# Kernel tuning notes

Hardware: AMD Instinct MI355X
Metric: run time of the kernel (lower is better)

The kernel has to match this reference:

```python
import jax, jax.numpy as jnp
import numpy as np

HEADS = 8


def setup_inputs() -> dict:
    key = jax.random.key(0)
    ks = jax.random.split(key, 7)
    b, t, e, h = 4, 2048, 128, HEADS
    x = jax.random.normal(ks[0], (b, t, e), dtype=jnp.float32)
    mask = jax.random.randint(ks[1], (1, t, t), 0, 2, dtype=jnp.int32)
    Wq = jax.random.normal(ks[2], (e, e * h), dtype=jnp.float32) / np.sqrt(e)
    Wk = jax.random.normal(ks[3], (e, e * h), dtype=jnp.float32) / np.sqrt(e)
    Wv = jax.random.normal(ks[4], (e, e * h), dtype=jnp.float32) / np.sqrt(e)
    Wu = jax.random.normal(ks[5], (e * h, e), dtype=jnp.float32) / np.sqrt(e * h)
    bu = jax.random.normal(ks[6], (e,), dtype=jnp.float32) * 0.01
    return {"x": x, "mask": mask, "Wq": Wq, "Wk": Wk, "Wv": Wv, "Wu": Wu, "bu": bu}


def reference(x, mask, Wq, Wk, Wv, Wu, bu):
    b, t, e = x.shape
    h = HEADS
    scale = e ** (-0.25)  # original scales q and k each by e**(1/4)
    # project and split heads: (b, t, h, e) -> (b, h, t, e)
    q = (x @ Wq).reshape(b, t, h, e).transpose(0, 2, 1, 3) * scale
    k = (x @ Wk).reshape(b, t, h, e).transpose(0, 2, 1, 3) * scale
    v = (x @ Wv).reshape(b, t, h, e).transpose(0, 2, 1, 3)
    dot = jnp.einsum('bhqe,bhke->bhqk', q, k)  # (b, h, t, t)
    # causal mask: strictly-upper triangle set to -inf (mask_diagonal=False -> offset=1)
    causal = jnp.triu(jnp.ones((t, t), dtype=bool), k=1)
    dot = jnp.where(causal, jnp.float32(-np.inf), dot)
    # external mask: positions where mask == 0 set to -1e9 (broadcast over b*h)
    dot = jnp.where((mask == 0)[:, None, :, :], jnp.float32(-1e9), dot)
    att = jax.nn.softmax(dot, axis=-1)
    out = jnp.einsum('bhqk,bhke->bhqe', att, v)
    out = out.transpose(0, 2, 1, 3).reshape(b, t, h * e)
    return out @ Wu + bu
```

## Files before the change

### kernel.cpp

```cpp
#include <hip/hip_runtime.h>
#include <hip/hip_bf16.h>

typedef unsigned short u16;
typedef unsigned int u32;
typedef __attribute__((ext_vector_type(8))) short bf16x8;
typedef __attribute__((ext_vector_type(4))) float f32x4;
typedef __attribute__((ext_vector_type(8))) unsigned short u16x8;
typedef __attribute__((ext_vector_type(2))) unsigned int u32x2;

#define T_ 2048
#define H_ 8
#define BH_ 32
#define M_ 8192
#define SCALE_QK 0.29730177875068026f
#define LOG2E 1.4426950408889634f

__device__ __forceinline__ u16 f2bf(float f) {
  union { __hip_bfloat16 h; u16 u; } cv; cv.h = __float2bfloat16(f); return cv.u;
}
__device__ __forceinline__ float bf2f(u16 u) {
  union { u16 u; __hip_bfloat16 h; } cv; cv.u = u; return __bfloat162float(cv.h);
}


__global__ __launch_bounds__(256)
void prep_kernel(const float* __restrict__ x, const float* __restrict__ Wq,
                 const float* __restrict__ Wk, const float* __restrict__ Wv,
                 const float* __restrict__ Wu,
                 u16* __restrict__ xb, u16* __restrict__ WT, u16* __restrict__ WuT)
{
  int i = blockIdx.x * 256 + threadIdx.x;
  if (i < M_ * 128) { xb[i] = f2bf(x[i]); return; }
  int j = i - M_ * 128;
  if (j < 3072 * 128) {
    int n = j >> 7, k = j & 127;
    float w;
    if (n < 1024)      w = Wq[k * 1024 + n] * (SCALE_QK * LOG2E);
    else if (n < 2048) w = Wk[k * 1024 + (n - 1024)] * SCALE_QK;
    else               w = Wv[k * 1024 + (n - 2048)];
    WT[j] = f2bf(w);
    return;
  }
  int u = j - 3072 * 128;
  if (u < 128 * 1024) {
    int n = u >> 10, k = u & 1023;
    WuT[u] = f2bf(Wu[k * 128 + n]);
  }
}

__global__ __launch_bounds__(256)
void maskprep_kernel(const int* __restrict__ mask, u32* __restrict__ mbits,
                     u32* __restrict__ deglist, u32* __restrict__ degcount,
                     float* __restrict__ cnt0inv)
{
  int wave = threadIdx.x >> 6, lane = threadIdx.x & 63;
  int q = blockIdx.x * 4 + wave;
  const int* row = mask + (long)q * 2048;
  unsigned long long anyvis = 0ull;
  int cnt1 = 0;
  for (int it = 0; it < 32; ++it) {
    int k = it * 64 + lane;
    unsigned long long bal = __ballot(row[k] != 0);
    if (lane == 0) {
      mbits[q * 64 + it * 2]     = (u32)bal;
      mbits[q * 64 + it * 2 + 1] = (u32)(bal >> 32);
    }
    cnt1 += __popcll(bal);
    int lim = q - it * 64;
    if (lim >= 63)      anyvis |= bal;
    else if (lim >= 0)  anyvis |= (bal & ((2ull << lim) - 1ull));
  }
  if (lane == 0) {
    int c0 = 2048 - cnt1;
    cnt0inv[q] = (c0 > 0) ? 1.0f / (float)c0 : 0.0f;
    if (anyvis == 0ull) {
      u32 slot = atomicAdd(degcount, 1u);
      deglist[slot] = (u32)q;
    }
  }
}

__global__ __launch_bounds__(256)
void qkv_kernel(const u16* __restrict__ xb, const u16* __restrict__ WT,
                u16* __restrict__ Qb, u16* __restrict__ Kimg, u16* __restrict__ Vimg)
{
  __shared__ __align__(16) u16 As[128 * 128];
  __shared__ __align__(16) u16 Bs[128 * 128];
  const int tid = threadIdx.x;
  const int n0 = blockIdx.x * 128;
  const int m0 = blockIdx.y * 128;
#pragma unroll
  for (int i = 0; i < 8; ++i) {
    int c = tid + 256 * i;
    int row = c >> 4, d0 = (c & 15) * 8;
    int soff = row * 128 + ((((d0 >> 3)) ^ (row & 15)) << 3);
    *(u16x8*)(&As[soff]) = *(const u16x8*)(&xb[(m0 + row) * 128 + d0]);
    *(u16x8*)(&Bs[soff]) = *(const u16x8*)(&WT[(n0 + row) * 128 + d0]);
  }
  __syncthreads();
  const int wave = tid >> 6, lane = tid & 63;
  const int lr = lane & 15, lg = lane >> 4;
  const int wm = (wave >> 1) * 64, wn = (wave & 1) * 64;
  f32x4 acc[4][4];
#pragma unroll
  for (int a = 0; a < 4; ++a)
#pragma unroll
    for (int b = 0; b < 4; ++b) acc[a][b] = (f32x4){0.f, 0.f, 0.f, 0.f};
#pragma unroll
  for (int ks = 0; ks < 4; ++ks) {
    bf16x8 af[4], bf[4];
#pragma unroll
    for (int mt = 0; mt < 4; ++mt) {
      int row = wm + mt * 16 + lr, chunk = lg + ks * 4;
      af[mt] = *(const bf16x8*)(&As[row * 128 + ((chunk ^ (row & 15)) << 3)]);
    }
#pragma unroll
    for (int nt = 0; nt < 4; ++nt) {
      int row = wn + nt * 16 + lr, chunk = lg + ks * 4;
      bf[nt] = *(const bf16x8*)(&Bs[row * 128 + ((chunk ^ (row & 15)) << 3)]);
    }
#pragma unroll
    for (int mt = 0; mt < 4; ++mt)
#pragma unroll
      for (int nt = 0; nt < 4; ++nt)
        acc[mt][nt] = __builtin_amdgcn_mfma_f32_16x16x32_bf16(af[mt], bf[nt], acc[mt][nt], 0, 0, 0);
  }
  const int mat = n0 >> 10;
  const int hh = (n0 & 1023) >> 7;
  const int bb = m0 >> 11;
  const long bhb = (long)(bb * H_ + hh);
  __syncthreads();
  if (mat != 2) {
#pragma unroll
    for (int mt = 0; mt < 4; ++mt)
#pragma unroll
      for (int nt = 0; nt < 4; ++nt)
#pragma unroll
        for (int r = 0; r < 4; ++r) {
          int tl = wm + mt * 16 + lg * 4 + r;
          int d  = wn + nt * 16 + lr;
          As[tl * 128 + ((((d >> 3)) ^ (tl & 15)) << 3) + (d & 7)] = f2bf(acc[mt][nt][r]);
        }
    __syncthreads();
    if (mat == 0) {
#pragma unroll
      for (int i = 0; i < 8; ++i) {
        int c = tid + 256 * i;
        int row = c >> 4, d0 = (c & 15) * 8;
        u16x8 v = *(const u16x8*)(&As[row * 128 + ((((d0 >> 3)) ^ (row & 15)) << 3)]);
        *(u16x8*)(&Qb[(bhb * T_ + ((m0 + row) & 2047)) * 128 + d0]) = v;
      }
    } else {
#pragma unroll
      for (int i = 0; i < 8; ++i) {
        int c = tid + 256 * i;
        int row = c >> 4, d0 = (c & 15) * 8;
        u16x8 v = *(const u16x8*)(&As[row * 128 + ((((d0 >> 3)) ^ (row & 15)) << 3)]);
        int t = (m0 + row) & 2047;
        int kt = t >> 6, kr = t & 63;
        *(u16x8*)(&Kimg[(bhb * 32 + kt) * 8192 + kr * 128 + ((((d0 >> 3)) ^ (kr & 15)) << 3)]) = v;
      }
    }
  } else {
    u16* TT = As;
#pragma unroll
    for (int mt = 0; mt < 4; ++mt)
#pragma unroll
      for (int nt = 0; nt < 4; ++nt)
#pragma unroll
        for (int r = 0; r < 4; ++r) {
          int tl = wm + mt * 16 + lg * 4 + r;
          int d  = wn + nt * 16 + lr;
          TT[d * 128 + ((((tl >> 3)) ^ (d & 15)) << 3) + (tl & 7)] = f2bf(acc[mt][nt][r]);
        }
    __syncthreads();
    const int tg0 = m0 & 2047;
#pragma unroll
    for (int i = 0; i < 8; ++i) {
      int c = tid + 256 * i;
      int d = c >> 4, t0 = (c & 15) * 8;
      u16x8 v = *(const u16x8*)(&TT[d * 128 + ((((t0 >> 3)) ^ (d & 15)) << 3)]);
      int tg = tg0 + t0;
      int kt = tg >> 6, kk = tg & 63;
      *(u16x8*)(&Vimg[(bhb * 32 + kt) * 8192 + d * 64 + (((kk >> 3) ^ (d & 7)) << 3)]) = v;
    }
  }
}

__global__ __launch_bounds__(256, 3)
void flash_kernel(const u16* __restrict__ Qb, const u16* __restrict__ Kimg,
                  const u16* __restrict__ Vimg, const u32* __restrict__ mbits,
                  u16* __restrict__ Ob)
{
  __shared__ __align__(16) u16 Ks[64 * 128];
  __shared__ __align__(16) u16 VTs[128 * 64];
  __shared__ __align__(16) u16 Ps[4][16 * 64];
  const int tid = threadIdx.x;
  const int g = blockIdx.x >> 5;
  const int a_ = g & 7, quad = g >> 3;
  const int qt = (quad == 0) ? (31 - a_) : (quad == 1) ? (8 + a_)
               : (quad == 2) ? (23 - a_) : a_;
  const int bh = blockIdx.x & 31;
  const int q0 = qt * 64;
  const int wave = tid >> 6, lane = tid & 63;
  const int lr = lane & 15, lg = lane >> 4;
  const long base = (long)bh * T_ * 128;
  const long iblk = (long)bh * 32;
  const int ldsoff = wave * 2048 + lane * 8;
  const int qrl = wave * 16 + lr;
  const int swz = (lr & 7) << 1;

  bf16x8 qf[4];
  {
    const u16* qrow = Qb + base + (long)(q0 + qrl) * 128;
#pragma unroll
    for (int ks = 0; ks < 4; ++ks)
      qf[ks] = *(const bf16x8*)(&qrow[lg * 8 + ks * 32]);
  }
  f32x4 acc[8];
#pragma unroll
  for (int i = 0; i < 8; ++i) acc[i] = (f32x4){0.f, 0.f, 0.f, 0.f};
  float mrun = -__builtin_inff(), lrun = 0.f;

  u16x8 kreg[4], vreg[4];
  {
    const u16* ks0 = Kimg + iblk * 8192 + ldsoff;
    const u16* vs0 = Vimg + iblk * 8192 + ldsoff;
#pragma unroll
    for (int i = 0; i < 4; ++i) {
      kreg[i] = *(const u16x8*)(ks0 + i * 512);
      vreg[i] = *(const u16x8*)(vs0 + i * 512);
    }
  }

  for (int kt = 0; kt <= qt; ++kt) {
    __syncthreads();
#pragma unroll
    for (int i = 0; i < 4; ++i) {
      *(u16x8*)(&Ks[ldsoff + i * 512]) = kreg[i];
      *(u16x8*)(&VTs[ldsoff + i * 512]) = vreg[i];
    }
    __syncthreads();
    if (kt < qt) {
      const u16* ksn = Kimg + (iblk + kt + 1) * 8192 + ldsoff;
      const u16* vsn = Vimg + (iblk + kt + 1) * 8192 + ldsoff;
#pragma unroll
      for (int i = 0; i < 4; ++i) {
        kreg[i] = *(const u16x8*)(ksn + i * 512);
        vreg[i] = *(const u16x8*)(vsn + i * 512);
      }
    }
    u32 mw0, mw1;
    {
      const u32* mp = &mbits[(q0 + qrl) * 64 + kt * 2];
      mw0 = mp[0]; mw1 = mp[1];
    }

    f32x4 s[4];
    __builtin_amdgcn_s_setprio(1);
#pragma unroll
    for (int ft = 0; ft < 4; ++ft) {
      f32x4 sa = (f32x4){0.f, 0.f, 0.f, 0.f};
#pragma unroll
      for (int ks = 0; ks < 4; ++ks) {
        int kr = ft * 16 + lr, chunk = lg + ks * 4;
        bf16x8 kf = *(const bf16x8*)(&Ks[kr * 128 + ((chunk ^ (kr & 15)) << 3)]);
        sa = __builtin_amdgcn_mfma_f32_16x16x32_bf16(kf, qf[ks], sa, 0, 0, 0);
      }
      s[ft] = sa;
    }
    __builtin_amdgcn_s_setprio(0);
    const bool diag = (kt == qt);
#pragma unroll
    for (int ft = 0; ft < 4; ++ft) {
      u32 w = (ft & 2) ? mw1 : mw0;
      int kbase = ft * 16 + lg * 4;
      int sh = ((ft & 1) << 4) + lg * 4;
#pragma unroll
      for (int r = 0; r < 4; ++r) {
        bool vis = (w >> (sh + r)) & 1u;
        if (diag && (kbase + r) > qrl) vis = false;
        if (!vis) s[ft][r] = -__builtin_inff();
      }
    }
    float t0 = fmaxf(fmaxf(s[0][0], s[0][1]), fmaxf(s[0][2], s[0][3]));
    float t1 = fmaxf(fmaxf(s[1][0], s[1][1]), fmaxf(s[1][2], s[1][3]));
    float t2 = fmaxf(fmaxf(s[2][0], s[2][1]), fmaxf(s[2][2], s[2][3]));
    float t3 = fmaxf(fmaxf(s[3][0], s[3][1]), fmaxf(s[3][2], s[3][3]));
    float tm = fmaxf(fmaxf(t0, t1), fmaxf(t2, t3));
    tm = fmaxf(tm, __shfl_xor(tm, 16));
    tm = fmaxf(tm, __shfl_xor(tm, 32));
    const bool skip = __all(tm - mrun <= 8.0f);
    float fac = 1.0f;
    float msafe = (mrun == -__builtin_inff()) ? 0.f : mrun;
    if (!skip) {
      float mnew = fmaxf(mrun, tm);
      msafe = (mnew == -__builtin_inff()) ? 0.f : mnew;
      fac = __builtin_amdgcn_exp2f(mrun - msafe);
      mrun = mnew;
    }
    float rs = 0.f;
#pragma unroll
    for (int ft = 0; ft < 4; ++ft) {
      float p0 = __builtin_amdgcn_exp2f(s[ft][0] - msafe);
      float p1 = __builtin_amdgcn_exp2f(s[ft][1] - msafe);
      float p2 = __builtin_amdgcn_exp2f(s[ft][2] - msafe);
      float p3 = __builtin_amdgcn_exp2f(s[ft][3] - msafe);
      s[ft][0] = p0; s[ft][1] = p1; s[ft][2] = p2; s[ft][3] = p3;
      rs += (p0 + p1) + (p2 + p3);
    }
    rs += __shfl_xor(rs, 16);
    rs += __shfl_xor(rs, 32);
    lrun = lrun * fac + rs;
    if (!skip) {
#pragma unroll
      for (int nt = 0; nt < 8; ++nt)
#pragma unroll
        for (int r = 0; r < 4; ++r) acc[nt][r] *= fac;
    }
#pragma unroll
    for (int ft = 0; ft < 4; ++ft) {
      u16 h0 = f2bf(s[ft][0]), h1 = f2bf(s[ft][1]);
      u16 h2 = f2bf(s[ft][2]), h3 = f2bf(s[ft][3]);
      u32x2 pw; pw[0] = (u32)h0 | ((u32)h1 << 16); pw[1] = (u32)h2 | ((u32)h3 << 16);
      int ch4 = (ft * 4 + lg) ^ swz;
      *(u32x2*)(&Ps[wave][lr * 64 + ch4 * 4]) = pw;
    }
    bf16x8 pa[2];
#pragma unroll
    for (int s2 = 0; s2 < 2; ++s2) {
      int ch4b = (s2 * 8 + lg * 2) ^ swz;
      pa[s2] = *(const bf16x8*)(&Ps[wave][lr * 64 + ch4b * 4]);
    }
    __builtin_amdgcn_s_setprio(1);
#pragma unroll
    for (int nt = 0; nt < 8; ++nt)
#pragma unroll
      for (int s2 = 0; s2 < 2; ++s2) {
        int d = nt * 16 + lr, chunk = lg + s2 * 4;
        bf16x8 vf = *(const bf16x8*)(&VTs[d * 64 + ((chunk ^ (d & 7)) << 3)]);
        acc[nt] = __builtin_amdgcn_mfma_f32_16x16x32_bf16(vf, pa[s2], acc[nt], 0, 0, 0);
      }
    __builtin_amdgcn_s_setprio(0);
  }
  const float inv = (lrun > 0.f) ? 1.f / lrun : 0.f;
  const long orow = base + (long)(q0 + qrl) * 128;
#pragma unroll
  for (int nt = 0; nt < 8; ++nt) {
    u16 h0 = f2bf(acc[nt][0] * inv), h1 = f2bf(acc[nt][1] * inv);
    u16 h2 = f2bf(acc[nt][2] * inv), h3 = f2bf(acc[nt][3] * inv);
    u32x2 ow; ow[0] = (u32)h0 | ((u32)h1 << 16); ow[1] = (u32)h2 | ((u32)h3 << 16);
    *(u32x2*)(&Ob[orow + nt * 16 + lg * 4]) = ow;
  }
}

__global__ __launch_bounds__(256)
void fixup_partial_kernel(const u32* __restrict__ deglist, const u32* __restrict__ degcount,
                          const u32* __restrict__ mbits, const u16* __restrict__ Vimg,
                          float* __restrict__ partial)
{
  const int slot = blockIdx.z;
  const u32 cnt = *degcount;
  if (slot >= (int)cnt) return;
  const int ksec = blockIdx.x, bh = blockIdx.y;
  const int q = (int)deglist[slot];
  const int t = threadIdx.x;
  const int d = t & 127, kc = t >> 7;
  const u16* vb = Vimg + ((long)bh * 32 + ksec) * 8192 + d * 64;
  const u32 w0 = mbits[q * 64 + ksec * 2];
  const u32 w1 = mbits[q * 64 + ksec * 2 + 1];
  float a = 0.f;
#pragma unroll
  for (int i = 0; i < 4; ++i) {
    int c = kc * 4 + i;
    u32 bits = ((kc == 0) ? (w0 >> (c * 8)) : (w1 >> ((c - 4) * 8))) & 0xffu;
    u16x8 v = *(const u16x8*)(&vb[(c ^ (d & 7)) << 3]);
#pragma unroll
    for (int j = 0; j < 8; ++j)
      a += ((bits >> j) & 1u) ? 0.f : bf2f(v[j]);
  }
  __shared__ float tmp[2][128];
  tmp[kc][d] = a;
  __syncthreads();
  if (t < 128)
    partial[(((long)slot * BH_ + bh) * 128 + d) * 32 + ksec] = tmp[0][d] + tmp[1][d];
}

__global__ __launch_bounds__(128)
void fixup_combine_kernel(const u32* __restrict__ deglist, const u32* __restrict__ degcount,
                          const float* __restrict__ cnt0inv, const float* __restrict__ partial,
                          u16* __restrict__ Ob)
{
  const int slot = blockIdx.x;
  const u32 cnt = *degcount;
  if (slot >= (int)cnt) return;
  const int bh = blockIdx.y;
  const int q = (int)deglist[slot];
  const int d = threadIdx.x;
  const float* p = partial + (((long)slot * BH_ + bh) * 128 + d) * 32;
  float s = 0.f;
#pragma unroll
  for (int i = 0; i < 8; ++i) {
    f32x4 v = *(const f32x4*)(&p[i * 4]);
    s += (v[0] + v[1]) + (v[2] + v[3]);
  }
  Ob[((long)bh * T_ + q) * 128 + d] = f2bf(s * cnt0inv[q]);
}

__global__ __launch_bounds__(256)
void fixup_slow_kernel(const u32* __restrict__ deglist, const u32* __restrict__ degcount,
                       const float* __restrict__ cnt0inv, const u32* __restrict__ mbits,
                       const u16* __restrict__ Vimg, u16* __restrict__ Ob)
{
  const u32 cnt = *degcount;
  const int bh = blockIdx.y;
  const int d = threadIdx.x & 127, half = threadIdx.x >> 7;
  __shared__ float tmp[2][128];
  const u16* vb = Vimg + (long)bh * 32 * 8192;
  for (u32 idx = 8 + blockIdx.x; idx < cnt; idx += gridDim.x) {
    const int q = (int)deglist[idx];
    const float inv = cnt0inv[q];
    float a = 0.f;
#pragma unroll 16
    for (int i = 0; i < 128; ++i) {
      int k0 = half * 1024 + i * 8;
      u32 w = mbits[q * 64 + (k0 >> 5)];
      u32 bits = (w >> (k0 & 31)) & 0xffu;
      int kt = k0 >> 6, kk = k0 & 63;
      u16x8 v = *(const u16x8*)(&vb[(long)kt * 8192 + d * 64 + (((kk >> 3) ^ (d & 7)) << 3)]);
#pragma unroll
      for (int j = 0; j < 8; ++j)
        a += ((bits >> j) & 1u) ? 0.f : bf2f(v[j]);
    }
    tmp[half][d] = a;
    __syncthreads();
    if (half == 0)
      Ob[((long)bh * T_ + q) * 128 + d] = f2bf((tmp[0][d] + tmp[1][d]) * inv);
    __syncthreads();
  }
}

__global__ __launch_bounds__(256)
void outproj_kernel(const u16* __restrict__ Ob, const u16* __restrict__ WuT,
                    const float* __restrict__ bu, float* __restrict__ out)
{
  __shared__ __align__(16) u16 As[32 * 128];
  __shared__ __align__(16) u16 Bs[128 * 128];
  const int tid = threadIdx.x;
  const int m0 = blockIdx.x * 32;
  const int wave = tid >> 6, lane = tid & 63;
  const int lr = lane & 15, lg = lane >> 4;
  f32x4 acc[2][2];
#pragma unroll
  for (int a = 0; a < 2; ++a)
#pragma unroll
    for (int b = 0; b < 2; ++b) acc[a][b] = (f32x4){0.f, 0.f, 0.f, 0.f};
  for (int kc = 0; kc < 8; ++kc) {
    __syncthreads();
#pragma unroll
    for (int i = 0; i < 2; ++i) {
      int c = tid + 256 * i;
      int row = c >> 4, d0 = (c & 15) * 8;
      int m = m0 + row, bb = m >> 11, t = m & 2047;
      *(u16x8*)(&As[row * 128 + ((((d0 >> 3)) ^ (row & 15)) << 3)]) =
          *(const u16x8*)(&Ob[((long)(bb * H_ + kc) * T_ + t) * 128 + d0]);
    }
#pragma unroll
    for (int i = 0; i < 8; ++i) {
      int c = tid + 256 * i;
      int row = c >> 4, d0 = (c & 15) * 8;
      *(u16x8*)(&Bs[row * 128 + ((((d0 >> 3)) ^ (row & 15)) << 3)]) =
          *(const u16x8*)(&WuT[row * 1024 + kc * 128 + d0]);
    }
    __syncthreads();
#pragma unroll
    for (int ks = 0; ks < 4; ++ks) {
      bf16x8 af[2], bf2[2];
#pragma unroll
      for (int mt = 0; mt < 2; ++mt) {
        int row = mt * 16 + lr, chunk = lg + ks * 4;
        af[mt] = *(const bf16x8*)(&As[row * 128 + ((chunk ^ (row & 15)) << 3)]);
      }
#pragma unroll
      for (int nt = 0; nt < 2; ++nt) {
        int row = wave * 32 + nt * 16 + lr, chunk = lg + ks * 4;
        bf2[nt] = *(const bf16x8*)(&Bs[row * 128 + ((chunk ^ (row & 15)) << 3)]);
      }
#pragma unroll
      for (int mt = 0; mt < 2; ++mt)
#pragma unroll
        for (int nt = 0; nt < 2; ++nt)
          acc[mt][nt] = __builtin_amdgcn_mfma_f32_16x16x32_bf16(af[mt], bf2[nt], acc[mt][nt], 0, 0, 0);
    }
  }
#pragma unroll
  for (int mt = 0; mt < 2; ++mt)
#pragma unroll
    for (int nt = 0; nt < 2; ++nt) {
      int n = wave * 32 + nt * 16 + lr;
      float bias = bu[n];
#pragma unroll
      for (int r = 0; r < 4; ++r) {
        int m = m0 + mt * 16 + lg * 4 + r;
        out[(long)m * 128 + n] = acc[mt][nt][r] + bias;
      }
    }
}

extern "C" void kernel_launch(void* const* d_in, const int* in_sizes, int n_in,
                              void* d_out, int out_size, void* d_ws, size_t ws_size,
                              hipStream_t stream)
{
  (void)in_sizes; (void)n_in; (void)out_size; (void)ws_size;
  const float* x   = (const float*)d_in[0];
  const int*   msk = (const int*)d_in[1];
  const float* Wq  = (const float*)d_in[2];
  const float* Wk  = (const float*)d_in[3];
  const float* Wv  = (const float*)d_in[4];
  const float* Wu  = (const float*)d_in[5];
  const float* bu  = (const float*)d_in[6];
  float* out = (float*)d_out;

  u16* Qb   = (u16*)d_ws;
  u16* Kimg = Qb + (size_t)BH_ * T_ * 128;
  u16* Vimg = Kimg + (size_t)BH_ * T_ * 128;
  u16* Obf  = Vimg + (size_t)BH_ * T_ * 128;
  u16* xb   = Obf + (size_t)BH_ * T_ * 128;
  u16* WT   = xb + (size_t)M_ * 128;
  u16* WuT  = WT + (size_t)3072 * 128;
  u32* mbits   = (u32*)(WuT + (size_t)128 * 1024);
  u32* deglist = mbits + (size_t)2048 * 64;
  u32* degcount = deglist + 2048;
  float* cnt0inv = (float*)(degcount + 1);
  float* partial = (float*)Qb;

  hipMemsetAsync(degcount, 0, sizeof(u32), stream);
  prep_kernel<<<6144, 256, 0, stream>>>(x, Wq, Wk, Wv, Wu, xb, WT, WuT);
  maskprep_kernel<<<512, 256, 0, stream>>>(msk, mbits, deglist, degcount, cnt0inv);
  qkv_kernel<<<dim3(24, 64), 256, 0, stream>>>(xb, WT, Qb, Kimg, Vimg);
  flash_kernel<<<1024, 256, 0, stream>>>(Qb, Kimg, Vimg, mbits, Obf);
  fixup_partial_kernel<<<dim3(32, 32, 8), 256, 0, stream>>>(deglist, degcount, mbits, Vimg, partial);
  fixup_combine_kernel<<<dim3(8, 32), 128, 0, stream>>>(deglist, degcount, cnt0inv, partial, Obf);
  fixup_slow_kernel<<<dim3(32, 32), 256, 0, stream>>>(deglist, degcount, cnt0inv, mbits, Vimg, Obf);
  outproj_kernel<<<256, 256, 0, stream>>>(Obf, WuT, bu, out);
}
```

Measured before the change: 133.5 us.

## Double query rows per flash block to reuse K/V tiles across two row groups

Each flash block now handles 128 query rows instead of 64: every wave keeps two 16-row query groups (A and B), each with its own online-softmax state, and runs both against each K/V tile loaded into shared memory. The grid is halved to 512 blocks and the causal tile scheduling is remapped with a pairing scheme. The goal is to halve global K/V loads and syncs per query row and to interleave independent MFMA chains. In exchange, register pressure roughly doubles (occupancy hint lowered from 3 to 2), the diagonal region wastes more masked work, and fewer blocks may hurt load balance.

```diff
diff --git a/kernel.cpp b/kernel.cpp
--- a/kernel.cpp
+++ b/kernel.cpp
@@ -187,7 +187,7 @@
   }
 }
 
-__global__ __launch_bounds__(256, 3)
+__global__ __launch_bounds__(256, 2)
 void flash_kernel(const u16* __restrict__ Qb, const u16* __restrict__ Kimg,
                   const u16* __restrict__ Vimg, const u32* __restrict__ mbits,
                   u16* __restrict__ Ob)
@@ -197,30 +197,37 @@
   __shared__ __align__(16) u16 Ps[4][16 * 64];
   const int tid = threadIdx.x;
   const int g = blockIdx.x >> 5;
-  const int a_ = g & 7, quad = g >> 3;
-  const int qt = (quad == 0) ? (31 - a_) : (quad == 1) ? (8 + a_)
-               : (quad == 2) ? (23 - a_) : a_;
+  const int qt = (g < 8) ? g : (23 - g);
   const int bh = blockIdx.x & 31;
-  const int q0 = qt * 64;
+  const int q0 = qt * 128;
   const int wave = tid >> 6, lane = tid & 63;
   const int lr = lane & 15, lg = lane >> 4;
   const long base = (long)bh * T_ * 128;
   const long iblk = (long)bh * 32;
   const int ldsoff = wave * 2048 + lane * 8;
-  const int qrl = wave * 16 + lr;
+  const int qrlA = wave * 32 + lr;
+  const int qrlB = qrlA + 16;
   const int swz = (lr & 7) << 1;
-
-  bf16x8 qf[4];
+  const int nkt = 2 * qt + 2;
+
+  bf16x8 qfA[4], qfB[4];
   {
-    const u16* qrow = Qb + base + (long)(q0 + qrl) * 128;
-#pragma unroll
-    for (int ks = 0; ks < 4; ++ks)
-      qf[ks] = *(const bf16x8*)(&qrow[lg * 8 + ks * 32]);
-  }
-  f32x4 acc[8];
-#pragma unroll
-  for (int i = 0; i < 8; ++i) acc[i] = (f32x4){0.f, 0.f, 0.f, 0.f};
-  float mrun = -__builtin_inff(), lrun = 0.f;
+    const u16* qa = Qb + base + (long)(q0 + qrlA) * 128;
+    const u16* qb = Qb + base + (long)(q0 + qrlB) * 128;
+#pragma unroll
+    for (int ks = 0; ks < 4; ++ks) {
+      qfA[ks] = *(const bf16x8*)(&qa[lg * 8 + ks * 32]);
+      qfB[ks] = *(const bf16x8*)(&qb[lg * 8 + ks * 32]);
+    }
+  }
+  f32x4 accA[8], accB[8];
+#pragma unroll
+  for (int i = 0; i < 8; ++i) {
+    accA[i] = (f32x4){0.f, 0.f, 0.f, 0.f};
+    accB[i] = (f32x4){0.f, 0.f, 0.f, 0.f};
+  }
+  float mrunA = -__builtin_inff(), lrunA = 0.f;
+  float mrunB = -__builtin_inff(), lrunB = 0.f;
 
   u16x8 kreg[4], vreg[4];
   {
@@ -233,7 +240,7 @@
     }
   }
 
-  for (int kt = 0; kt <= qt; ++kt) {
+  for (int kt = 0; kt < nkt; ++kt) {
     __syncthreads();
 #pragma unroll
     for (int i = 0; i < 4; ++i) {
@@ -241,7 +248,7 @@
       *(u16x8*)(&VTs[ldsoff + i * 512]) = vreg[i];
     }
     __syncthreads();
-    if (kt < qt) {
+    if (kt + 1 < nkt) {
       const u16* ksn = Kimg + (iblk + kt + 1) * 8192 + ldsoff;
       const u16* vsn = Vimg + (iblk + kt + 1) * 8192 + ldsoff;
 #pragma unroll
@@ -250,87 +257,151 @@
         vreg[i] = *(const u16x8*)(vsn + i * 512);
       }
     }
-    u32 mw0, mw1;
+    u32 mwA0, mwA1, mwB0, mwB1;
     {
-      const u32* mp = &mbits[(q0 + qrl) * 64 + kt * 2];
-      mw0 = mp[0]; mw1 = mp[1];
-    }
-
-    f32x4 s[4];
+      const u32* mpA = &mbits[(q0 + qrlA) * 64 + kt * 2];
+      const u32* mpB = &mbits[(q0 + qrlB) * 64 + kt * 2];
+      mwA0 = mpA[0]; mwA1 = mpA[1];
+      mwB0 = mpB[0]; mwB1 = mpB[1];
+    }
+
+    f32x4 sA[4], sB[4];
     __builtin_amdgcn_s_setprio(1);
 #pragma unroll
     for (int ft = 0; ft < 4; ++ft) {
-      f32x4 sa = (f32x4){0.f, 0.f, 0.f, 0.f};
+      f32x4 a = (f32x4){0.f, 0.f, 0.f, 0.f};
+      f32x4 b = (f32x4){0.f, 0.f, 0.f, 0.f};
 #pragma unroll
       for (int ks = 0; ks < 4; ++ks) {
         int kr = ft * 16 + lr, chunk = lg + ks * 4;
         bf16x8 kf = *(const bf16x8*)(&Ks[kr * 128 + ((chunk ^ (kr & 15)) << 3)]);
-        sa = __builtin_amdgcn_mfma_f32_16x16x32_bf16(kf, qf[ks], sa, 0, 0, 0);
-      }
-      s[ft] = sa;
+        a = __builtin_amdgcn_mfma_f32_16x16x32_bf16(kf, qfA[ks], a, 0, 0, 0);
+        b = __builtin_amdgcn_mfma_f32_16x16x32_bf16(kf, qfB[ks], b, 0, 0, 0);
+      }
+      sA[ft] = a; sB[ft] = b;
     }
     __builtin_amdgcn_s_setprio(0);
-    const bool diag = (kt == qt);
+    const bool diag = (kt >= 2 * qt);
+    const int kv0 = kt * 64;
 #pragma unroll
     for (int ft = 0; ft < 4; ++ft) {
-      u32 w = (ft & 2) ? mw1 : mw0;
+      u32 wA = (ft & 2) ? mwA1 : mwA0;
+      u32 wB = (ft & 2) ? mwB1 : mwB0;
       int kbase = ft * 16 + lg * 4;
       int sh = ((ft & 1) << 4) + lg * 4;
 #pragma unroll
       for (int r = 0; r < 4; ++r) {
-        bool vis = (w >> (sh + r)) & 1u;
-        if (diag && (kbase + r) > qrl) vis = false;
-        if (!vis) s[ft][r] = -__builtin_inff();
-      }
-    }
-    float t0 = fmaxf(fmaxf(s[0][0], s[0][1]), fmaxf(s[0][2], s[0][3]));
-    float t1 = fmaxf(fmaxf(s[1][0], s[1][1]), fmaxf(s[1][2], s[1][3]));
-    float t2 = fmaxf(fmaxf(s[2][0], s[2][1]), fmaxf(s[2][2], s[2][3]));
-    float t3 = fmaxf(fmaxf(s[3][0], s[3][1]), fmaxf(s[3][2], s[3][3]));
-    float tm = fmaxf(fmaxf(t0, t1), fmaxf(t2, t3));
-    tm = fmaxf(tm, __shfl_xor(tm, 16));
-    tm = fmaxf(tm, __shfl_xor(tm, 32));
-    const bool skip = __all(tm - mrun <= 8.0f);
-    float fac = 1.0f;
-    float msafe = (mrun == -__builtin_inff()) ? 0.f : mrun;
-    if (!skip) {
-      float mnew = fmaxf(mrun, tm);
-      msafe = (mnew == -__builtin_inff()) ? 0.f : mnew;
-      fac = __builtin_amdgcn_exp2f(mrun - msafe);
-      mrun = mnew;
-    }
-    float rs = 0.f;
+        bool visA = (wA >> (sh + r)) & 1u;
+        bool visB = (wB >> (sh + r)) & 1u;
+        if (diag) {
+          int key = kv0 + kbase + r;
+          if (key > q0 + qrlA) visA = false;
+          if (key > q0 + qrlB) visB = false;
+        }
+        if (!visA) sA[ft][r] = -__builtin_inff();
+        if (!visB) sB[ft][r] = -__builtin_inff();
+      }
+    }
+    {
+      float t0 = fmaxf(fmaxf(sA[0][0], sA[0][1]), fmaxf(sA[0][2], sA[0][3]));
+      float t1 = fmaxf(fmaxf(sA[1][0], sA[1][1]), fmaxf(sA[1][2], sA[1][3]));
+      float t2 = fmaxf(fmaxf(sA[2][0], sA[2][1]), fmaxf(sA[2][2], sA[2][3]));
+      float t3 = fmaxf(fmaxf(sA[3][0], sA[3][1]), fmaxf(sA[3][2], sA[3][3]));
+      float tm = fmaxf(fmaxf(t0, t1), fmaxf(t2, t3));
+      tm = fmaxf(tm, __shfl_xor(tm, 16));
+      tm = fmaxf(tm, __shfl_xor(tm, 32));
+      const bool skip = __all(tm - mrunA <= 8.0f);
+      float fac = 1.0f;
+      float msafe = (mrunA == -__builtin_inff()) ? 0.f : mrunA;
+      if (!skip) {
+        float mnew = fmaxf(mrunA, tm);
+        msafe = (mnew == -__builtin_inff()) ? 0.f : mnew;
+        fac = __builtin_amdgcn_exp2f(mrunA - msafe);
+        mrunA = mnew;
+      }
+      float rs = 0.f;
+#pragma unroll
+      for (int ft = 0; ft < 4; ++ft) {
+        float p0 = __builtin_amdgcn_exp2f(sA[ft][0] - msafe);
+        float p1 = __builtin_amdgcn_exp2f(sA[ft][1] - msafe);
+        float p2 = __builtin_amdgcn_exp2f(sA[ft][2] - msafe);
+        float p3 = __builtin_amdgcn_exp2f(sA[ft][3] - msafe);
+        sA[ft][0] = p0; sA[ft][1] = p1; sA[ft][2] = p2; sA[ft][3] = p3;
+        rs += (p0 + p1) + (p2 + p3);
+      }
+      rs += __shfl_xor(rs, 16);
+      rs += __shfl_xor(rs, 32);
+      lrunA = lrunA * fac + rs;
+      if (!skip) {
+#pragma unroll
+        for (int nt = 0; nt < 8; ++nt)
+#pragma unroll
+          for (int r = 0; r < 4; ++r) accA[nt][r] *= fac;
+      }
+    }
+    {
+      float t0 = fmaxf(fmaxf(sB[0][0], sB[0][1]), fmaxf(sB[0][2], sB[0][3]));
+      float t1 = fmaxf(fmaxf(sB[1][0], sB[1][1]), fmaxf(sB[1][2], sB[1][3]));
+      float t2 = fmaxf(fmaxf(sB[2][0], sB[2][1]), fmaxf(sB[2][2], sB[2][3]));
+      float t3 = fmaxf(fmaxf(sB[3][0], sB[3][1]), fmaxf(sB[3][2], sB[3][3]));
+      float tm = fmaxf(fmaxf(t0, t1), fmaxf(t2, t3));
+      tm = fmaxf(tm, __shfl_xor(tm, 16));
+      tm = fmaxf(tm, __shfl_xor(tm, 32));
+      const bool skip = __all(tm - mrunB <= 8.0f);
+      float fac = 1.0f;
+      float msafe = (mrunB == -__builtin_inff()) ? 0.f : mrunB;
+      if (!skip) {
+        float mnew = fmaxf(mrunB, tm);
+        msafe = (mnew == -__builtin_inff()) ? 0.f : mnew;
+        fac = __builtin_amdgcn_exp2f(mrunB - msafe);
+        mrunB = mnew;
+      }
+      float rs = 0.f;
+#pragma unroll
+      for (int ft = 0; ft < 4; ++ft) {
+        float p0 = __builtin_amdgcn_exp2f(sB[ft][0] - msafe);
+        float p1 = __builtin_amdgcn_exp2f(sB[ft][1] - msafe);
+        float p2 = __builtin_amdgcn_exp2f(sB[ft][2] - msafe);
+        float p3 = __builtin_amdgcn_exp2f(sB[ft][3] - msafe);
+        sB[ft][0] = p0; sB[ft][1] = p1; sB[ft][2] = p2; sB[ft][3] = p3;
+        rs += (p0 + p1) + (p2 + p3);
+      }
+      rs += __shfl_xor(rs, 16);
+      rs += __shfl_xor(rs, 32);
+      lrunB = lrunB * fac + rs;
+      if (!skip) {
+#pragma unroll
+        for (int nt = 0; nt < 8; ++nt)
+#pragma unroll
+          for (int r = 0; r < 4; ++r) accB[nt][r] *= fac;
+      }
+    }
+    bf16x8 paA[2], paB[2];
 #pragma unroll
     for (int ft = 0; ft < 4; ++ft) {
-      float p0 = __builtin_amdgcn_exp2f(s[ft][0] - msafe);
-      float p1 = __builtin_amdgcn_exp2f(s[ft][1] - msafe);
-      float p2 = __builtin_amdgcn_exp2f(s[ft][2] - msafe);
-      float p3 = __builtin_amdgcn_exp2f(s[ft][3] - msafe);
-      s[ft][0] = p0; s[ft][1] = p1; s[ft][2] = p2; s[ft][3] = p3;
-      rs += (p0 + p1) + (p2 + p3);
-    }
-    rs += __shfl_xor(rs, 16);
-    rs += __shfl_xor(rs, 32);
-    lrun = lrun * fac + rs;
-    if (!skip) {
-#pragma unroll
-      for (int nt = 0; nt < 8; ++nt)
-#pragma unroll
-        for (int r = 0; r < 4; ++r) acc[nt][r] *= fac;
-    }
-#pragma unroll
-    for (int ft = 0; ft < 4; ++ft) {
-      u16 h0 = f2bf(s[ft][0]), h1 = f2bf(s[ft][1]);
-      u16 h2 = f2bf(s[ft][2]), h3 = f2bf(s[ft][3]);
+      u16 h0 = f2bf(sA[ft][0]), h1 = f2bf(sA[ft][1]);
+      u16 h2 = f2bf(sA[ft][2]), h3 = f2bf(sA[ft][3]);
       u32x2 pw; pw[0] = (u32)h0 | ((u32)h1 << 16); pw[1] = (u32)h2 | ((u32)h3 << 16);
       int ch4 = (ft * 4 + lg) ^ swz;
       *(u32x2*)(&Ps[wave][lr * 64 + ch4 * 4]) = pw;
     }
-    bf16x8 pa[2];
 #pragma unroll
     for (int s2 = 0; s2 < 2; ++s2) {
       int ch4b = (s2 * 8 + lg * 2) ^ swz;
-      pa[s2] = *(const bf16x8*)(&Ps[wave][lr * 64 + ch4b * 4]);
+      paA[s2] = *(const bf16x8*)(&Ps[wave][lr * 64 + ch4b * 4]);
+    }
+#pragma unroll
+    for (int ft = 0; ft < 4; ++ft) {
+      u16 h0 = f2bf(sB[ft][0]), h1 = f2bf(sB[ft][1]);
+      u16 h2 = f2bf(sB[ft][2]), h3 = f2bf(sB[ft][3]);
+      u32x2 pw; pw[0] = (u32)h0 | ((u32)h1 << 16); pw[1] = (u32)h2 | ((u32)h3 << 16);
+      int ch4 = (ft * 4 + lg) ^ swz;
+      *(u32x2*)(&Ps[wave][lr * 64 + ch4 * 4]) = pw;
+    }
+#pragma unroll
+    for (int s2 = 0; s2 < 2; ++s2) {
+      int ch4b = (s2 * 8 + lg * 2) ^ swz;
+      paB[s2] = *(const bf16x8*)(&Ps[wave][lr * 64 + ch4b * 4]);
     }
     __builtin_amdgcn_s_setprio(1);
 #pragma unroll
@@ -339,18 +410,25 @@
       for (int s2 = 0; s2 < 2; ++s2) {
         int d = nt * 16 + lr, chunk = lg + s2 * 4;
         bf16x8 vf = *(const bf16x8*)(&VTs[d * 64 + ((chunk ^ (d & 7)) << 3)]);
-        acc[nt] = __builtin_amdgcn_mfma_f32_16x16x32_bf16(vf, pa[s2], acc[nt], 0, 0, 0);
+        accA[nt] = __builtin_amdgcn_mfma_f32_16x16x32_bf16(vf, paA[s2], accA[nt], 0, 0, 0);
+        accB[nt] = __builtin_amdgcn_mfma_f32_16x16x32_bf16(vf, paB[s2], accB[nt], 0, 0, 0);
       }
     __builtin_amdgcn_s_setprio(0);
   }
-  const float inv = (lrun > 0.f) ? 1.f / lrun : 0.f;
-  const long orow = base + (long)(q0 + qrl) * 128;
+  const float invA = (lrunA > 0.f) ? 1.f / lrunA : 0.f;
+  const float invB = (lrunB > 0.f) ? 1.f / lrunB : 0.f;
+  const long orowA = base + (long)(q0 + qrlA) * 128;
+  const long orowB = base + (long)(q0 + qrlB) * 128;
 #pragma unroll
   for (int nt = 0; nt < 8; ++nt) {
-    u16 h0 = f2bf(acc[nt][0] * inv), h1 = f2bf(acc[nt][1] * inv);
-    u16 h2 = f2bf(acc[nt][2] * inv), h3 = f2bf(acc[nt][3] * inv);
-    u32x2 ow; ow[0] = (u32)h0 | ((u32)h1 << 16); ow[1] = (u32)h2 | ((u32)h3 << 16);
-    *(u32x2*)(&Ob[orow + nt * 16 + lg * 4]) = ow;
+    u16 a0 = f2bf(accA[nt][0] * invA), a1 = f2bf(accA[nt][1] * invA);
+    u16 a2 = f2bf(accA[nt][2] * invA), a3 = f2bf(accA[nt][3] * invA);
+    u32x2 owA; owA[0] = (u32)a0 | ((u32)a1 << 16); owA[1] = (u32)a2 | ((u32)a3 << 16);
+    *(u32x2*)(&Ob[orowA + nt * 16 + lg * 4]) = owA;
+    u16 b0 = f2bf(accB[nt][0] * invB), b1 = f2bf(accB[nt][1] * invB);
+    u16 b2 = f2bf(accB[nt][2] * invB), b3 = f2bf(accB[nt][3] * invB);
+    u32x2 owB; owB[0] = (u32)b0 | ((u32)b1 << 16); owB[1] = (u32)b2 | ((u32)b3 << 16);
+    *(u32x2*)(&Ob[orowB + nt * 16 + lg * 4]) = owB;
   }
 }
 
@@ -538,7 +616,7 @@
   prep_kernel<<<6144, 256, 0, stream>>>(x, Wq, Wk, Wv, Wu, xb, WT, WuT);
   maskprep_kernel<<<512, 256, 0, stream>>>(msk, mbits, deglist, degcount, cnt0inv);
   qkv_kernel<<<dim3(24, 64), 256, 0, stream>>>(xb, WT, Qb, Kimg, Vimg);
-  flash_kernel<<<1024, 256, 0, stream>>>(Qb, Kimg, Vimg, mbits, Obf);
+  flash_kernel<<<512, 256, 0, stream>>>(Qb, Kimg, Vimg, mbits, Obf);
   fixup_partial_kernel<<<dim3(32, 32, 8), 256, 0, stream>>>(deglist, degcount, mbits, Vimg, partial);
   fixup_combine_kernel<<<dim3(8, 32), 128, 0, stream>>>(deglist, degcount, cnt0inv, partial, Obf);
   fixup_slow_kernel<<<dim3(32, 32), 256, 0, stream>>>(deglist, degcount, cnt0inv, mbits, Vimg, Obf);
```

Measured after the change: 160.3 us. 20.1% more time.
